# Kernel tuning notes

Measured on AMD Instinct MI355X. Metric: run time of the kernel, lower is better.

Reference implementation:

```python
import jax, jax.numpy as jnp
import numpy as np

EPS = 1e-5
TAU = 2.0
HEADS = 8
SCALE = 0.125


def _bn(y, g, b, m, v):
    # y: [TB, C, N]; per-channel eval-mode batchnorm
    inv = jax.lax.rsqrt(v + EPS)
    return (y - m[:, None]) * (g * inv)[:, None] + b[:, None]


def _lif(x_seq, vth):
    # spikingjelly MultiStepLIFNode: v += (x - v)/tau, spike = H(v - vth), hard reset v*(1-s)
    def step(mem, xt):
        mem = mem + (xt - mem) / TAU
        s = (mem >= vth).astype(xt.dtype)
        mem = mem * (1.0 - s)
        return mem, s
    _, spikes = jax.lax.scan(step, jnp.zeros_like(x_seq[0]), x_seq)
    return spikes


def setup_inputs() -> dict:
    key = jax.random.key(0)
    ks = jax.random.split(key, 8)
    T, B, C, H, W = 4, 16, 256, 32, 32
    d = {
        'x': jax.random.normal(ks[0], (T, B, C, H, W), jnp.float32),
        'res_attn': jnp.zeros((1,), jnp.float32),
    }
    for i, p in enumerate(['q', 'k', 'v']):
        d[p + '_w'] = jax.random.normal(ks[1 + i], (C, C), jnp.float32) * 0.02
        d[p + '_gamma'] = jnp.ones((C,), jnp.float32)
        d[p + '_beta'] = jnp.zeros((C,), jnp.float32)
        d[p + '_mean'] = jnp.zeros((C,), jnp.float32)
        d[p + '_var'] = jnp.ones((C,), jnp.float32)
    d['p_w'] = jax.random.normal(ks[4], (C, C), jnp.float32) * 0.02
    d['p_b'] = jnp.zeros((C,), jnp.float32)
    d['p_gamma'] = jnp.ones((C,), jnp.float32)
    d['p_beta'] = jnp.zeros((C,), jnp.float32)
    d['p_mean'] = jnp.zeros((C,), jnp.float32)
    d['p_var'] = jnp.ones((C,), jnp.float32)
    return d


def reference(x, res_attn, q_w, q_gamma, q_beta, q_mean, q_var,
              k_w, k_gamma, k_beta, k_mean, k_var,
              v_w, v_gamma, v_beta, v_mean, v_var,
              p_w, p_b, p_gamma, p_beta, p_mean, p_var):
    T, B, C, H, W = x.shape
    N = H * W
    d = C // HEADS
    x2 = x.reshape(T * B, C, N)

    def branch(w, g, b, m, v):
        y = _bn(jnp.einsum('oc,bcn->bon', w, x2), g, b, m, v).reshape(T, B, C, N)
        s = _lif(y, 1.0)  # [T,B,C,N]
        # -> [T,B,heads,N,d]
        return s.transpose(0, 1, 3, 2).reshape(T, B, N, HEADS, d).transpose(0, 1, 3, 2, 4)

    q = branch(q_w, q_gamma, q_beta, q_mean, q_var)
    k = branch(k_w, k_gamma, k_beta, k_mean, k_var)
    v = branch(v_w, v_gamma, v_beta, v_mean, v_var)

    kv = jnp.einsum('tbhnd,tbhne->tbhde', k, v)      # [T,B,h,d,d]
    attn = jnp.einsum('tbhnd,tbhde->tbhne', q, kv) * SCALE  # [T,B,h,N,d]
    xa = attn.transpose(0, 1, 2, 4, 3).reshape(T, B, C, N)
    xa = _lif(xa, 0.5)

    y = _bn(jnp.einsum('oc,bcn->bon', p_w, xa.reshape(T * B, C, N)) + p_b[:, None],
            p_gamma, p_beta, p_mean, p_var)
    out = _lif(y.reshape(T, B, C, H, W), 1.0)
    return (out, v)
```

## Files before the change

kernel.cpp:

```cpp
#include <hip/hip_runtime.h>
#include <stdint.h>

typedef unsigned int u32;
typedef unsigned short ushort_t;

#define T_ 4
#define B_ 16
#define C_ 256
#define N_ 1024
#define CN (C_ * N_)
#define M_ELEMS (64 * C_ * N_)

#define OFF_S    0ull
#define OFF_XC   67108864ull
#define OFF_SC   67108864ull
#define OFF_KV   134217728ull
#define OFF_BNS  136314880ull
#define OFF_WC   136331264ull
#define OFF_WPC  137510912ull

typedef __attribute__((ext_vector_type(8))) short bf16x8;
typedef __attribute__((ext_vector_type(4))) float f32x4;

#define SWZ(c) (((c) & ~3) | (((c) & 3) ^ (((c) >> 2) & 3) ^ (((c) >> 4) & 3)))

__device__ __forceinline__ ushort_t f2bf(float f) {
  u32 u = __float_as_uint(f);
  u32 r = (u + 0x7FFFu + ((u >> 16) & 1u)) >> 16;
  return (ushort_t)r;
}
__device__ __forceinline__ float bf2f(ushort_t h) { return __uint_as_float((u32)h << 16); }

__device__ __forceinline__ void async_copy16(const void* g, void* l) {
  __builtin_amdgcn_global_load_lds(
      (const __attribute__((address_space(1))) u32*)g,
      (__attribute__((address_space(3))) u32*)l, 16, 0, 0);
}

__device__ __forceinline__ void mfma_grp(const ushort_t* Ap, int aoff,
                                         bf16x8 b0, bf16x8 b1, bf16x8 b2, bf16x8 b3,
                                         f32x4* acc) {
  bf16x8 a0 = *(const bf16x8*)&Ap[aoff + 0 * 16 * 32];
  bf16x8 a1 = *(const bf16x8*)&Ap[aoff + 1 * 16 * 32];
  bf16x8 a2 = *(const bf16x8*)&Ap[aoff + 2 * 16 * 32];
  bf16x8 a3 = *(const bf16x8*)&Ap[aoff + 3 * 16 * 32];
  acc[0]  = __builtin_amdgcn_mfma_f32_16x16x32_bf16(a0, b0, acc[0],  0, 0, 0);
  acc[1]  = __builtin_amdgcn_mfma_f32_16x16x32_bf16(a0, b1, acc[1],  0, 0, 0);
  acc[2]  = __builtin_amdgcn_mfma_f32_16x16x32_bf16(a0, b2, acc[2],  0, 0, 0);
  acc[3]  = __builtin_amdgcn_mfma_f32_16x16x32_bf16(a0, b3, acc[3],  0, 0, 0);
  acc[4]  = __builtin_amdgcn_mfma_f32_16x16x32_bf16(a1, b0, acc[4],  0, 0, 0);
  acc[5]  = __builtin_amdgcn_mfma_f32_16x16x32_bf16(a1, b1, acc[5],  0, 0, 0);
  acc[6]  = __builtin_amdgcn_mfma_f32_16x16x32_bf16(a1, b2, acc[6],  0, 0, 0);
  acc[7]  = __builtin_amdgcn_mfma_f32_16x16x32_bf16(a1, b3, acc[7],  0, 0, 0);
  acc[8]  = __builtin_amdgcn_mfma_f32_16x16x32_bf16(a2, b0, acc[8],  0, 0, 0);
  acc[9]  = __builtin_amdgcn_mfma_f32_16x16x32_bf16(a2, b1, acc[9],  0, 0, 0);
  acc[10] = __builtin_amdgcn_mfma_f32_16x16x32_bf16(a2, b2, acc[10], 0, 0, 0);
  acc[11] = __builtin_amdgcn_mfma_f32_16x16x32_bf16(a2, b3, acc[11], 0, 0, 0);
  acc[12] = __builtin_amdgcn_mfma_f32_16x16x32_bf16(a3, b0, acc[12], 0, 0, 0);
  acc[13] = __builtin_amdgcn_mfma_f32_16x16x32_bf16(a3, b1, acc[13], 0, 0, 0);
  acc[14] = __builtin_amdgcn_mfma_f32_16x16x32_bf16(a3, b2, acc[14], 0, 0, 0);
  acc[15] = __builtin_amdgcn_mfma_f32_16x16x32_bf16(a3, b3, acc[15], 0, 0, 0);
}

__global__ void bn_prep(const float* __restrict__ qg, const float* __restrict__ qb2, const float* __restrict__ qm, const float* __restrict__ qv,
                        const float* __restrict__ kg, const float* __restrict__ kb, const float* __restrict__ km, const float* __restrict__ kvv,
                        const float* __restrict__ vg, const float* __restrict__ vb, const float* __restrict__ vm, const float* __restrict__ vv,
                        const float* __restrict__ pbias,
                        const float* __restrict__ pg, const float* __restrict__ pbt, const float* __restrict__ pm, const float* __restrict__ pv,
                        float* __restrict__ bns) {
  int i = threadIdx.x;
  int br = i >> 8, c = i & 255;
  const float *g, *bt, *m, *v;
  float bias = 0.f;
  if (br == 0)      { g = qg; bt = qb2; m = qm; v = qv; }
  else if (br == 1) { g = kg; bt = kb;  m = km; v = kvv; }
  else if (br == 2) { g = vg; bt = vb;  m = vm; v = vv; }
  else              { g = pg; bt = pbt; m = pm; v = pv; bias = pbias[c]; }
  float sc = g[c] / sqrtf(v[c] + 1e-5f);
  float sh = bt[c] + (bias - m[c]) * sc;
  float rcp = (sc != 0.f) ? (1.f / sc) : 0.f;
  *(float4*)&bns[4 * i] = make_float4(sc, sh, rcp, 0.f);
}

__global__ __launch_bounds__(256) void convert_w(const float* __restrict__ qw, const float* __restrict__ kw,
                                                 const float* __restrict__ vw, const float* __restrict__ pw,
                                                 ushort_t* __restrict__ Wc, ushort_t* __restrict__ Wpc) {
  int id = blockIdx.x * 256 + threadIdx.x;
  int br = id >> 16, o = (id >> 8) & 255, c = id & 255;
  const float* w = (br == 0) ? qw : (br == 1) ? kw : (br == 2) ? vw : pw;
  float f = w[o * 256 + c];
  ushort_t hi = f2bf(f);
  ushort_t lo = f2bf(f - bf2f(hi));
  if (br < 3) {
    ushort_t* d = Wc + (size_t)br * 196608 + (size_t)o * 768 + c;
    d[0] = hi; d[256] = lo; d[512] = hi;
  } else {
    ushort_t* d = Wpc + (size_t)o * 512 + c;
    d[0] = hi; d[256] = lo;
  }
}

__global__ __launch_bounds__(256) void convert_x(const float* __restrict__ x, ushort_t* __restrict__ Xc) {
  __shared__ ushort_t hi[32][260];
  __shared__ ushort_t lo[32][260];
  int bid = blockIdx.x;
  int nc = bid & 3, kb = (bid >> 2) & 7, tb = bid >> 5;
  int t = threadIdx.x;
  int n0 = nc * 256;
  const float* xb = x + (size_t)tb * CN + (size_t)(kb * 32) * N_ + n0;
#pragma unroll
  for (int p = 0; p < 8; ++p) {
    int k = p * 4 + (t >> 6);
    int n4 = (t & 63) * 4;
    float4 v = *(const float4*)&xb[(size_t)k * N_ + n4];
    ushort_t h0 = f2bf(v.x), h1 = f2bf(v.y), h2 = f2bf(v.z), h3 = f2bf(v.w);
    short4 hv = make_short4((short)h0, (short)h1, (short)h2, (short)h3);
    short4 lv = make_short4((short)f2bf(v.x - bf2f(h0)), (short)f2bf(v.y - bf2f(h1)),
                            (short)f2bf(v.z - bf2f(h2)), (short)f2bf(v.w - bf2f(h3)));
    *(short4*)&hi[k][n4] = hv;
    *(short4*)&lo[k][n4] = lv;
  }
  __syncthreads();
  ushort_t* Hs = Xc + ((size_t)(tb * 16 + kb) * 1024 + n0) * 32;
  ushort_t* Ls = Xc + ((size_t)(tb * 16 + 8 + kb) * 1024 + n0) * 32;
  int kq = t & 3;
#pragma unroll
  for (int q = 0; q < 4; ++q) {
    int n = q * 64 + (t >> 2);
    u32 a0 = (u32)hi[kq * 8 + 0][n] | ((u32)hi[kq * 8 + 1][n] << 16);
    u32 a1 = (u32)hi[kq * 8 + 2][n] | ((u32)hi[kq * 8 + 3][n] << 16);
    u32 a2 = (u32)hi[kq * 8 + 4][n] | ((u32)hi[kq * 8 + 5][n] << 16);
    u32 a3 = (u32)hi[kq * 8 + 6][n] | ((u32)hi[kq * 8 + 7][n] << 16);
    *(uint4*)(Hs + (size_t)n * 32 + kq * 8) = make_uint4(a0, a1, a2, a3);
    u32 b0 = (u32)lo[kq * 8 + 0][n] | ((u32)lo[kq * 8 + 1][n] << 16);
    u32 b1 = (u32)lo[kq * 8 + 2][n] | ((u32)lo[kq * 8 + 3][n] << 16);
    u32 b2 = (u32)lo[kq * 8 + 4][n] | ((u32)lo[kq * 8 + 5][n] << 16);
    u32 b3 = (u32)lo[kq * 8 + 6][n] | ((u32)lo[kq * 8 + 7][n] << 16);
    *(uint4*)(Ls + (size_t)n * 32 + kq * 8) = make_uint4(b0, b1, b2, b3);
  }
}

__global__ __launch_bounds__(256, 3) void gemm_qkv_lif(
    const ushort_t* __restrict__ Wc, const ushort_t* __restrict__ Xc,
    const float* __restrict__ bns, uint8_t* __restrict__ S) {
  __shared__ ushort_t Ah[2][4096];
  __shared__ ushort_t Xl[2][4096];
  __shared__ ushort_t Bh[2][4096];
  const int nt = blockIdx.x, mt = blockIdx.y, b = blockIdx.z;
  const int br = mt >> 1, rh = mt & 1;
  const ushort_t* Ab = Wc + (size_t)br * 196608 + (size_t)(rh * 128) * 768;
  const int tid = threadIdx.x;
  const int lane = tid & 63;
  const int quad = lane >> 4, r = lane & 15;
  const int w = tid >> 6;
  const int moff = (w & 1) * 64, noff = (w >> 1) * 64;
  const int c0 = tid, c1 = tid + 256;
  const int s0 = SWZ(c0), s1 = SWZ(c1);
  const int qx = quad ^ (r & 3) ^ ((r >> 2) & 3);
  const int aoff = (moff + r) * 32 + qx * 8;
  const int boff = (noff + r) * 32 + qx * 8;

  f32x4 acc[16];
#pragma unroll
  for (int f = 0; f < 16; ++f) acc[f] = (f32x4){0.f, 0.f, 0.f, 0.f};

  for (int t = 0; t < 4; ++t) {
    const ushort_t* Xtb = Xc + (size_t)(t * 16 + b) * 16 * 32768 + (size_t)(nt * 128) * 32;
    for (int p = 0; p < 4; ++p) {
      const ushort_t* AcH = Ab + p * 64;
      const ushort_t* AcL = Ab + 256 + p * 64;
      const ushort_t* Bh0 = Xtb + (size_t)(2 * p) * 32768;
      const ushort_t* Bh1 = Bh0 + 32768;
      async_copy16(AcH + (size_t)(c0 >> 2) * 768 + (s0 & 3) * 8,      &Ah[0][c0 * 8]);
      async_copy16(AcH + (size_t)(c1 >> 2) * 768 + (s1 & 3) * 8,      &Ah[0][c1 * 8]);
      async_copy16(AcH + (size_t)(c0 >> 2) * 768 + 32 + (s0 & 3) * 8, &Ah[1][c0 * 8]);
      async_copy16(AcH + (size_t)(c1 >> 2) * 768 + 32 + (s1 & 3) * 8, &Ah[1][c1 * 8]);
      async_copy16(AcL + (size_t)(c0 >> 2) * 768 + (s0 & 3) * 8,      &Xl[0][c0 * 8]);
      async_copy16(AcL + (size_t)(c1 >> 2) * 768 + (s1 & 3) * 8,      &Xl[0][c1 * 8]);
      async_copy16(AcL + (size_t)(c0 >> 2) * 768 + 32 + (s0 & 3) * 8, &Xl[1][c0 * 8]);
      async_copy16(AcL + (size_t)(c1 >> 2) * 768 + 32 + (s1 & 3) * 8, &Xl[1][c1 * 8]);
      async_copy16(Bh0 + s0 * 8, &Bh[0][c0 * 8]);
      async_copy16(Bh0 + s1 * 8, &Bh[0][c1 * 8]);
      async_copy16(Bh1 + s0 * 8, &Bh[1][c0 * 8]);
      async_copy16(Bh1 + s1 * 8, &Bh[1][c1 * 8]);
      __syncthreads();
      {
        bf16x8 b0 = *(const bf16x8*)&Bh[0][boff + 0 * 16 * 32];
        bf16x8 b1 = *(const bf16x8*)&Bh[0][boff + 1 * 16 * 32];
        bf16x8 b2 = *(const bf16x8*)&Bh[0][boff + 2 * 16 * 32];
        bf16x8 b3 = *(const bf16x8*)&Bh[0][boff + 3 * 16 * 32];
        mfma_grp(&Ah[0][0], aoff, b0, b1, b2, b3, acc);
        mfma_grp(&Xl[0][0], aoff, b0, b1, b2, b3, acc);
      }
      {
        bf16x8 b0 = *(const bf16x8*)&Bh[1][boff + 0 * 16 * 32];
        bf16x8 b1 = *(const bf16x8*)&Bh[1][boff + 1 * 16 * 32];
        bf16x8 b2 = *(const bf16x8*)&Bh[1][boff + 2 * 16 * 32];
        bf16x8 b3 = *(const bf16x8*)&Bh[1][boff + 3 * 16 * 32];
        mfma_grp(&Ah[1][0], aoff, b0, b1, b2, b3, acc);
        mfma_grp(&Xl[1][0], aoff, b0, b1, b2, b3, acc);
      }
      __syncthreads();
      const ushort_t* Bl0 = Xtb + (size_t)(8 + 2 * p) * 32768;
      const ushort_t* Bl1 = Bl0 + 32768;
      async_copy16(Bl0 + s0 * 8, &Xl[0][c0 * 8]);
      async_copy16(Bl0 + s1 * 8, &Xl[0][c1 * 8]);
      async_copy16(Bl1 + s0 * 8, &Xl[1][c0 * 8]);
      async_copy16(Bl1 + s1 * 8, &Xl[1][c1 * 8]);
      __syncthreads();
      {
        bf16x8 b0 = *(const bf16x8*)&Xl[0][boff + 0 * 16 * 32];
        bf16x8 b1 = *(const bf16x8*)&Xl[0][boff + 1 * 16 * 32];
        bf16x8 b2 = *(const bf16x8*)&Xl[0][boff + 2 * 16 * 32];
        bf16x8 b3 = *(const bf16x8*)&Xl[0][boff + 3 * 16 * 32];
        mfma_grp(&Ah[0][0], aoff, b0, b1, b2, b3, acc);
      }
      {
        bf16x8 b0 = *(const bf16x8*)&Xl[1][boff + 0 * 16 * 32];
        bf16x8 b1 = *(const bf16x8*)&Xl[1][boff + 1 * 16 * 32];
        bf16x8 b2 = *(const bf16x8*)&Xl[1][boff + 2 * 16 * 32];
        bf16x8 b3 = *(const bf16x8*)&Xl[1][boff + 3 * 16 * 32];
        mfma_grp(&Ah[1][0], aoff, b0, b1, b2, b3, acc);
      }
      __syncthreads();
    }
    uint8_t* Sb = S + (size_t)br * M_ELEMS + (size_t)(t * 16 + b) * CN;
#pragma unroll
    for (int i = 0; i < 4; ++i) {
#pragma unroll
      for (int rg = 0; rg < 4; ++rg) {
        int c = rh * 128 + moff + i * 16 + quad * 4 + rg;
        float4 bn = *(const float4*)&bns[4 * (br * 256 + c)];
        float hsc = 0.5f * bn.x;
        float hsh = 0.5f * bn.y;
        float rcp = bn.z;
        uint8_t* row = Sb + (size_t)c * N_ + nt * 128 + noff + r;
#pragma unroll
        for (int j = 0; j < 4; ++j) {
          float m = acc[i * 4 + j][rg] * hsc + hsh;
          uint8_t s = (m >= 1.0f) ? 1 : 0;
          row[j * 16] = s;
          acc[i * 4 + j][rg] = s ? 0.f : m * rcp;
        }
      }
    }
  }
}

__global__ __launch_bounds__(256) void kv_gram_tv(const uint8_t* __restrict__ SK,
                                                  const uint8_t* __restrict__ SV,
                                                  float* __restrict__ KV,
                                                  float* __restrict__ vout) {
  __shared__ unsigned long long Kb[32][17];
  __shared__ unsigned long long Vb[32][17];
  const int tb = blockIdx.x >> 3, h = blockIdx.x & 7;
  const uint8_t* K = SK + (size_t)tb * CN + (size_t)h * 32 * N_;
  const uint8_t* V = SV + (size_t)tb * CN + (size_t)h * 32 * N_;
  const int tid = threadIdx.x;
  const int row = tid >> 3, c8 = tid & 7;
  uint8_t* Kb8 = (uint8_t*)&Kb[row][0];
  uint8_t* Vb8 = (uint8_t*)&Vb[row][0];
#pragma unroll
  for (int i = 0; i < 16; ++i) {
    int c = c8 + 8 * i;
    unsigned long long xk = *(const unsigned long long*)(K + (size_t)row * N_ + (size_t)c * 8);
    unsigned long long xv = *(const unsigned long long*)(V + (size_t)row * N_ + (size_t)c * 8);
    Kb8[c] = (uint8_t)((xk * 0x8040201008040201ull) >> 56);
    Vb8[c] = (uint8_t)((xv * 0x8040201008040201ull) >> 56);
  }
  __syncthreads();
  {
    const int dd = tid >> 3, e0 = (tid & 7) * 4;
    int a0 = 0, a1 = 0, a2 = 0, a3 = 0;
#pragma unroll
    for (int c = 0; c < 16; ++c) {
      unsigned long long kd = Kb[dd][c];
      a0 += __popcll(kd & Vb[e0 + 0][c]);
      a1 += __popcll(kd & Vb[e0 + 1][c]);
      a2 += __popcll(kd & Vb[e0 + 2][c]);
      a3 += __popcll(kd & Vb[e0 + 3][c]);
    }
    float* o = KV + (size_t)(tb * 8 + h) * 1024 + dd * 32 + e0;
    o[0] = (float)a0; o[1] = (float)a1; o[2] = (float)a2; o[3] = (float)a3;
  }
  float* vo = vout + ((size_t)tb * 8 + h) * (size_t)(1024 * 32);
  const int sn = tid >> 3;
  const int dd0 = (tid & 7) * 4;
#pragma unroll 4
  for (int it = 0; it < 32; ++it) {
    int n = it * 32 + sn;
    int wi = n >> 6;
    int bit = ((n >> 3) & 7) * 8 + 7 - (n & 7);
    float4 v4;
    v4.x = ((Vb[dd0 + 0][wi] >> bit) & 1ull) ? 1.0f : 0.0f;
    v4.y = ((Vb[dd0 + 1][wi] >> bit) & 1ull) ? 1.0f : 0.0f;
    v4.z = ((Vb[dd0 + 2][wi] >> bit) & 1ull) ? 1.0f : 0.0f;
    v4.w = ((Vb[dd0 + 3][wi] >> bit) & 1ull) ? 1.0f : 0.0f;
    *(float4*)(vo + (size_t)n * 32 + dd0) = v4;
  }
}

__global__ __launch_bounds__(256) void attn_lif(const uint8_t* __restrict__ SQ,
                                                const float* __restrict__ KV,
                                                ushort_t* __restrict__ Sc) {
  __shared__ float kvs[1024];
  const int bid = blockIdx.x;
  const int nb = bid & 15, h = (bid >> 4) & 7, b = bid >> 7;
  const int n0 = nb * 64;
  const int tid = threadIdx.x;
  const int nl = tid & 63, eg = tid >> 6;
  float mem[8];
#pragma unroll
  for (int j = 0; j < 8; ++j) mem[j] = 0.f;
  for (int t = 0; t < 4; ++t) {
    const float* kvp = KV + (size_t)((t * B_ + b) * 8 + h) * 1024;
    *(float4*)&kvs[tid * 4] = *(const float4*)&kvp[tid * 4];
    __syncthreads();
    const uint8_t* q = SQ + (size_t)(t * B_ + b) * CN + (size_t)h * 32 * N_ + n0 + nl;
    float val[8];
#pragma unroll
    for (int j = 0; j < 8; ++j) val[j] = 0.f;
#pragma unroll 4
    for (int dd = 0; dd < 32; ++dd) {
      float qv = (float)q[(size_t)dd * N_];
      float4 ka = *(const float4*)&kvs[dd * 32 + eg * 8];
      float4 kb2 = *(const float4*)&kvs[dd * 32 + eg * 8 + 4];
      val[0] += qv * ka.x;  val[1] += qv * ka.y;  val[2] += qv * ka.z;  val[3] += qv * ka.w;
      val[4] += qv * kb2.x; val[5] += qv * kb2.y; val[6] += qv * kb2.z; val[7] += qv * kb2.w;
    }
    ushort_t pk[8];
#pragma unroll
    for (int j = 0; j < 8; ++j) {
      float a = val[j] * 0.125f;
      mem[j] += (a - mem[j]) * 0.5f;
      int s = (mem[j] >= 0.5f);
      pk[j] = s ? (ushort_t)0x3F80 : (ushort_t)0;
      if (s) mem[j] = 0.f;
    }
    uint4 o;
    o.x = (u32)pk[0] | ((u32)pk[1] << 16);
    o.y = (u32)pk[2] | ((u32)pk[3] << 16);
    o.z = (u32)pk[4] | ((u32)pk[5] << 16);
    o.w = (u32)pk[6] | ((u32)pk[7] << 16);
    *(uint4*)(Sc + ((size_t)((t * B_ + b) * 8 + h) * 1024 + n0 + nl) * 32 + eg * 8) = o;
    __syncthreads();
  }
}

__global__ __launch_bounds__(256, 3) void gemm_p_lif(
    const ushort_t* __restrict__ Wpc, const ushort_t* __restrict__ Sc,
    const float* __restrict__ bns, float* __restrict__ out) {
  __shared__ ushort_t Ah[2][4096];
  __shared__ ushort_t Al[2][4096];
  __shared__ ushort_t Bs[2][4096];
  const int nt = blockIdx.x, mt = blockIdx.y, b = blockIdx.z;
  const ushort_t* Ab = Wpc + (size_t)(mt * 128) * 512;
  const int tid = threadIdx.x;
  const int lane = tid & 63;
  const int quad = lane >> 4, r = lane & 15;
  const int w = tid >> 6;
  const int moff = (w & 1) * 64, noff = (w >> 1) * 64;
  const int c0 = tid, c1 = tid + 256;
  const int s0 = SWZ(c0), s1 = SWZ(c1);
  const int qx = quad ^ (r & 3) ^ ((r >> 2) & 3);
  const int aoff = (moff + r) * 32 + qx * 8;
  const int boff = (noff + r) * 32 + qx * 8;
  f32x4 acc[16];
#pragma unroll
  for (int f = 0; f < 16; ++f) acc[f] = (f32x4){0.f, 0.f, 0.f, 0.f};

  for (int t = 0; t < 4; ++t) {
    const ushort_t* Stb = Sc + (size_t)(t * 16 + b) * 8 * 32768 + (size_t)(nt * 128) * 32;
    for (int p = 0; p < 4; ++p) {
      const ushort_t* AcH = Ab + p * 64;
      const ushort_t* AcL = Ab + 256 + p * 64;
      const ushort_t* Bb0 = Stb + (size_t)(2 * p) * 32768;
      const ushort_t* Bb1 = Bb0 + 32768;
      async_copy16(AcH + (size_t)(c0 >> 2) * 512 + (s0 & 3) * 8,      &Ah[0][c0 * 8]);
      async_copy16(AcH + (size_t)(c1 >> 2) * 512 + (s1 & 3) * 8,      &Ah[0][c1 * 8]);
      async_copy16(AcH + (size_t)(c0 >> 2) * 512 + 32 + (s0 & 3) * 8, &Ah[1][c0 * 8]);
      async_copy16(AcH + (size_t)(c1 >> 2) * 512 + 32 + (s1 & 3) * 8, &Ah[1][c1 * 8]);
      async_copy16(AcL + (size_t)(c0 >> 2) * 512 + (s0 & 3) * 8,      &Al[0][c0 * 8]);
      async_copy16(AcL + (size_t)(c1 >> 2) * 512 + (s1 & 3) * 8,      &Al[0][c1 * 8]);
      async_copy16(AcL + (size_t)(c0 >> 2) * 512 + 32 + (s0 & 3) * 8, &Al[1][c0 * 8]);
      async_copy16(AcL + (size_t)(c1 >> 2) * 512 + 32 + (s1 & 3) * 8, &Al[1][c1 * 8]);
      async_copy16(Bb0 + s0 * 8, &Bs[0][c0 * 8]);
      async_copy16(Bb0 + s1 * 8, &Bs[0][c1 * 8]);
      async_copy16(Bb1 + s0 * 8, &Bs[1][c0 * 8]);
      async_copy16(Bb1 + s1 * 8, &Bs[1][c1 * 8]);
      __syncthreads();
      {
        bf16x8 b0 = *(const bf16x8*)&Bs[0][boff + 0 * 16 * 32];
        bf16x8 b1 = *(const bf16x8*)&Bs[0][boff + 1 * 16 * 32];
        bf16x8 b2 = *(const bf16x8*)&Bs[0][boff + 2 * 16 * 32];
        bf16x8 b3 = *(const bf16x8*)&Bs[0][boff + 3 * 16 * 32];
        mfma_grp(&Ah[0][0], aoff, b0, b1, b2, b3, acc);
        mfma_grp(&Al[0][0], aoff, b0, b1, b2, b3, acc);
      }
      {
        bf16x8 b0 = *(const bf16x8*)&Bs[1][boff + 0 * 16 * 32];
        bf16x8 b1 = *(const bf16x8*)&Bs[1][boff + 1 * 16 * 32];
        bf16x8 b2 = *(const bf16x8*)&Bs[1][boff + 2 * 16 * 32];
        bf16x8 b3 = *(const bf16x8*)&Bs[1][boff + 3 * 16 * 32];
        mfma_grp(&Ah[1][0], aoff, b0, b1, b2, b3, acc);
        mfma_grp(&Al[1][0], aoff, b0, b1, b2, b3, acc);
      }
      __syncthreads();
    }
    float* Ob = out + (size_t)(t * 16 + b) * CN;
#pragma unroll
    for (int i = 0; i < 4; ++i) {
#pragma unroll
      for (int rg = 0; rg < 4; ++rg) {
        int c = mt * 128 + moff + i * 16 + quad * 4 + rg;
        float4 bn = *(const float4*)&bns[4 * (768 + c)];
        float hsc = 0.5f * bn.x;
        float hsh = 0.5f * bn.y;
        float rcp = bn.z;
        float* row2 = Ob + (size_t)c * N_ + nt * 128 + noff + r;
#pragma unroll
        for (int j = 0; j < 4; ++j) {
          float m = acc[i * 4 + j][rg] * hsc + hsh;
          int s = (m >= 1.0f);
          row2[j * 16] = s ? 1.0f : 0.0f;
          acc[i * 4 + j][rg] = s ? 0.f : m * rcp;
        }
      }
    }
  }
}

extern "C" void kernel_launch(void* const* d_in, const int* in_sizes, int n_in,
                              void* d_out, int out_size, void* d_ws, size_t ws_size,
                              hipStream_t stream) {
  const float* x   = (const float*)d_in[0];
  const float* qw  = (const float*)d_in[2];
  const float* qg  = (const float*)d_in[3];
  const float* qb  = (const float*)d_in[4];
  const float* qm  = (const float*)d_in[5];
  const float* qv  = (const float*)d_in[6];
  const float* kw  = (const float*)d_in[7];
  const float* kg  = (const float*)d_in[8];
  const float* kb  = (const float*)d_in[9];
  const float* km  = (const float*)d_in[10];
  const float* kvv = (const float*)d_in[11];
  const float* vw  = (const float*)d_in[12];
  const float* vg  = (const float*)d_in[13];
  const float* vb  = (const float*)d_in[14];
  const float* vm  = (const float*)d_in[15];
  const float* vv  = (const float*)d_in[16];
  const float* pw  = (const float*)d_in[17];
  const float* pb  = (const float*)d_in[18];
  const float* pg  = (const float*)d_in[19];
  const float* pbt = (const float*)d_in[20];
  const float* pm  = (const float*)d_in[21];
  const float* pv  = (const float*)d_in[22];

  float* out = (float*)d_out;
  float* vout = out + M_ELEMS;

  uint8_t* ws = (uint8_t*)d_ws;
  uint8_t* S   = ws + OFF_S;
  ushort_t* Xc = (ushort_t*)(ws + OFF_XC);
  ushort_t* Sc = (ushort_t*)(ws + OFF_SC);
  float* KV    = (float*)(ws + OFF_KV);
  float* BNS   = (float*)(ws + OFF_BNS);
  ushort_t* Wc  = (ushort_t*)(ws + OFF_WC);
  ushort_t* Wpc = (ushort_t*)(ws + OFF_WPC);

  bn_prep<<<dim3(1), dim3(1024), 0, stream>>>(qg, qb, qm, qv, kg, kb, km, kvv,
                                              vg, vb, vm, vv, pb, pg, pbt, pm, pv, BNS);
  convert_w<<<dim3(1024), dim3(256), 0, stream>>>(qw, kw, vw, pw, Wc, Wpc);
  convert_x<<<dim3(2048), dim3(256), 0, stream>>>(x, Xc);
  gemm_qkv_lif<<<dim3(8, 6, 16), dim3(256), 0, stream>>>(Wc, Xc, BNS, S);
  kv_gram_tv<<<dim3(512), dim3(256), 0, stream>>>(S + 1ull * M_ELEMS, S + 2ull * M_ELEMS, KV, vout);
  attn_lif<<<dim3(2048), dim3(256), 0, stream>>>(S, KV, Sc);
  gemm_p_lif<<<dim3(8, 2, 16), dim3(256), 0, stream>>>(Wpc, Sc, BNS, out);
}
```

Baseline: 391.9 us.

## Load GEMM B operands directly from global into registers, merge prep kernels

In both MFMA GEMM kernels the B-operand (activation) tiles are now read straight from global memory into registers in the MFMA fragment layout instead of being staged through swizzled shared memory. This removes one LDS buffer and, in the QKV kernel, two extra barriers per k-step, and lets the global loads overlap with the MFMAs. The risk is less coalesced global access and no reuse of B across waves sharing the same columns. The bn_prep and convert_w kernels are also fused into one launch to save a kernel launch.

Measured after the change: 419.6 us. 7.1% more time.

```diff
diff --git a/kernel.cpp b/kernel.cpp
--- a/kernel.cpp
+++ b/kernel.cpp
@@ -62,41 +62,45 @@
   acc[15] = __builtin_amdgcn_mfma_f32_16x16x32_bf16(a3, b3, acc[15], 0, 0, 0);
 }
 
-__global__ void bn_prep(const float* __restrict__ qg, const float* __restrict__ qb2, const float* __restrict__ qm, const float* __restrict__ qv,
-                        const float* __restrict__ kg, const float* __restrict__ kb, const float* __restrict__ km, const float* __restrict__ kvv,
-                        const float* __restrict__ vg, const float* __restrict__ vb, const float* __restrict__ vm, const float* __restrict__ vv,
-                        const float* __restrict__ pbias,
-                        const float* __restrict__ pg, const float* __restrict__ pbt, const float* __restrict__ pm, const float* __restrict__ pv,
-                        float* __restrict__ bns) {
-  int i = threadIdx.x;
-  int br = i >> 8, c = i & 255;
-  const float *g, *bt, *m, *v;
-  float bias = 0.f;
-  if (br == 0)      { g = qg; bt = qb2; m = qm; v = qv; }
-  else if (br == 1) { g = kg; bt = kb;  m = km; v = kvv; }
-  else if (br == 2) { g = vg; bt = vb;  m = vm; v = vv; }
-  else              { g = pg; bt = pbt; m = pm; v = pv; bias = pbias[c]; }
-  float sc = g[c] / sqrtf(v[c] + 1e-5f);
-  float sh = bt[c] + (bias - m[c]) * sc;
-  float rcp = (sc != 0.f) ? (1.f / sc) : 0.f;
-  *(float4*)&bns[4 * i] = make_float4(sc, sh, rcp, 0.f);
-}
-
-__global__ __launch_bounds__(256) void convert_w(const float* __restrict__ qw, const float* __restrict__ kw,
-                                                 const float* __restrict__ vw, const float* __restrict__ pw,
-                                                 ushort_t* __restrict__ Wc, ushort_t* __restrict__ Wpc) {
-  int id = blockIdx.x * 256 + threadIdx.x;
-  int br = id >> 16, o = (id >> 8) & 255, c = id & 255;
-  const float* w = (br == 0) ? qw : (br == 1) ? kw : (br == 2) ? vw : pw;
-  float f = w[o * 256 + c];
-  ushort_t hi = f2bf(f);
-  ushort_t lo = f2bf(f - bf2f(hi));
-  if (br < 3) {
-    ushort_t* d = Wc + (size_t)br * 196608 + (size_t)o * 768 + c;
-    d[0] = hi; d[256] = lo; d[512] = hi;
+__global__ __launch_bounds__(256) void prep_w(
+    const float* __restrict__ qw, const float* __restrict__ kw,
+    const float* __restrict__ vw, const float* __restrict__ pw,
+    const float* __restrict__ qg, const float* __restrict__ qb2, const float* __restrict__ qm, const float* __restrict__ qv,
+    const float* __restrict__ kg, const float* __restrict__ kb, const float* __restrict__ km, const float* __restrict__ kvv,
+    const float* __restrict__ vg, const float* __restrict__ vb, const float* __restrict__ vm, const float* __restrict__ vv,
+    const float* __restrict__ pbias, const float* __restrict__ pg, const float* __restrict__ pbt,
+    const float* __restrict__ pm, const float* __restrict__ pv,
+    ushort_t* __restrict__ Wc, ushort_t* __restrict__ Wpc, float* __restrict__ bns) {
+  if (blockIdx.x < 1024) {
+    int id = blockIdx.x * 256 + threadIdx.x;
+    int br = id >> 16, o = (id >> 8) & 255, c = id & 255;
+    const float* w = (br == 0) ? qw : (br == 1) ? kw : (br == 2) ? vw : pw;
+    float f = w[o * 256 + c];
+    ushort_t hi = f2bf(f);
+    ushort_t lo = f2bf(f - bf2f(hi));
+    if (br < 3) {
+      ushort_t* d = Wc + (size_t)br * 196608 + (size_t)o * 768 + c;
+      d[0] = hi; d[256] = lo; d[512] = hi;
+    } else {
+      ushort_t* d = Wpc + (size_t)o * 512 + c;
+      d[0] = hi; d[256] = lo;
+    }
   } else {
-    ushort_t* d = Wpc + (size_t)o * 512 + c;
-    d[0] = hi; d[256] = lo;
+#pragma unroll
+    for (int rep = 0; rep < 4; ++rep) {
+      int i = rep * 256 + threadIdx.x;
+      int br = i >> 8, c = i & 255;
+      const float *g, *bt, *m, *v;
+      float bias = 0.f;
+      if (br == 0)      { g = qg; bt = qb2; m = qm; v = qv; }
+      else if (br == 1) { g = kg; bt = kb;  m = km; v = kvv; }
+      else if (br == 2) { g = vg; bt = vb;  m = vm; v = vv; }
+      else              { g = pg; bt = pbt; m = pm; v = pv; bias = pbias[c]; }
+      float sc = g[c] / sqrtf(v[c] + 1e-5f);
+      float sh = bt[c] + (bias - m[c]) * sc;
+      float rcp = (sc != 0.f) ? (1.f / sc) : 0.f;
+      *(float4*)&bns[4 * i] = make_float4(sc, sh, rcp, 0.f);
+    }
   }
 }
 
@@ -144,8 +148,7 @@
     const ushort_t* __restrict__ Wc, const ushort_t* __restrict__ Xc,
     const float* __restrict__ bns, uint8_t* __restrict__ S) {
   __shared__ ushort_t Ah[2][4096];
-  __shared__ ushort_t Xl[2][4096];
-  __shared__ ushort_t Bh[2][4096];
+  __shared__ ushort_t Al[2][4096];
   const int nt = blockIdx.x, mt = blockIdx.y, b = blockIdx.z;
   const int br = mt >> 1, rh = mt & 1;
   const ushort_t* Ab = Wc + (size_t)br * 196608 + (size_t)(rh * 128) * 768;
@@ -158,7 +161,7 @@
   const int s0 = SWZ(c0), s1 = SWZ(c1);
   const int qx = quad ^ (r & 3) ^ ((r >> 2) & 3);
   const int aoff = (moff + r) * 32 + qx * 8;
-  const int boff = (noff + r) * 32 + qx * 8;
+  const int bro = (noff + r) * 32 + quad * 8;
 
   f32x4 acc[16];
 #pragma unroll
@@ -169,59 +172,41 @@
     for (int p = 0; p < 4; ++p) {
       const ushort_t* AcH = Ab + p * 64;
       const ushort_t* AcL = Ab + 256 + p * 64;
-      const ushort_t* Bh0 = Xtb + (size_t)(2 * p) * 32768;
-      const ushort_t* Bh1 = Bh0 + 32768;
       async_copy16(AcH + (size_t)(c0 >> 2) * 768 + (s0 & 3) * 8,      &Ah[0][c0 * 8]);
       async_copy16(AcH + (size_t)(c1 >> 2) * 768 + (s1 & 3) * 8,      &Ah[0][c1 * 8]);
       async_copy16(AcH + (size_t)(c0 >> 2) * 768 + 32 + (s0 & 3) * 8, &Ah[1][c0 * 8]);
       async_copy16(AcH + (size_t)(c1 >> 2) * 768 + 32 + (s1 & 3) * 8, &Ah[1][c1 * 8]);
-      async_copy16(AcL + (size_t)(c0 >> 2) * 768 + (s0 & 3) * 8,      &Xl[0][c0 * 8]);
-      async_copy16(AcL + (size_t)(c1 >> 2) * 768 + (s1 & 3) * 8,      &Xl[0][c1 * 8]);
-      async_copy16(AcL + (size_t)(c0 >> 2) * 768 + 32 + (s0 & 3) * 8, &Xl[1][c0 * 8]);
-      async_copy16(AcL + (size_t)(c1 >> 2) * 768 + 32 + (s1 & 3) * 8, &Xl[1][c1 * 8]);
-      async_copy16(Bh0 + s0 * 8, &Bh[0][c0 * 8]);
-      async_copy16(Bh0 + s1 * 8, &Bh[0][c1 * 8]);
-      async_copy16(Bh1 + s0 * 8, &Bh[1][c0 * 8]);
-      async_copy16(Bh1 + s1 * 8, &Bh[1][c1 * 8]);
+      async_copy16(AcL + (size_t)(c0 >> 2) * 768 + (s0 & 3) * 8,      &Al[0][c0 * 8]);
+      async_copy16(AcL + (size_t)(c1 >> 2) * 768 + (s1 & 3) * 8,      &Al[0][c1 * 8]);
+      async_copy16(AcL + (size_t)(c0 >> 2) * 768 + 32 + (s0 & 3) * 8, &Al[1][c0 * 8]);
+      async_copy16(AcL + (size_t)(c1 >> 2) * 768 + 32 + (s1 & 3) * 8, &Al[1][c1 * 8]);
+      const ushort_t* B0 = Xtb + (size_t)(2 * p) * 32768 + bro;
+      const ushort_t* B1 = B0 + 32768;
+      const ushort_t* B2 = Xtb + (size_t)(8 + 2 * p) * 32768 + bro;
+      const ushort_t* B3 = B2 + 32768;
+      bf16x8 gA0 = *(const bf16x8*)(B0 + 0 * 512);
+      bf16x8 gA1 = *(const bf16x8*)(B0 + 1 * 512);
+      bf16x8 gA2 = *(const bf16x8*)(B0 + 2 * 512);
+      bf16x8 gA3 = *(const bf16x8*)(B0 + 3 * 512);
       __syncthreads();
-      {
-        bf16x8 b0 = *(const bf16x8*)&Bh[0][boff + 0 * 16 * 32];
-        bf16x8 b1 = *(const bf16x8*)&Bh[0][boff + 1 * 16 * 32];
-        bf16x8 b2 = *(const bf16x8*)&Bh[0][boff + 2 * 16 * 32];
-        bf16x8 b3 = *(const bf16x8*)&Bh[0][boff + 3 * 16 * 32];
-        mfma_grp(&Ah[0][0], aoff, b0, b1, b2, b3, acc);
-        mfma_grp(&Xl[0][0], aoff, b0, b1, b2, b3, acc);
-      }
-      {
-        bf16x8 b0 = *(const bf16x8*)&Bh[1][boff + 0 * 16 * 32];
-        bf16x8 b1 = *(const bf16x8*)&Bh[1][boff + 1 * 16 * 32];
-        bf16x8 b2 = *(const bf16x8*)&Bh[1][boff + 2 * 16 * 32];
-        bf16x8 b3 = *(const bf16x8*)&Bh[1][boff + 3 * 16 * 32];
-        mfma_grp(&Ah[1][0], aoff, b0, b1, b2, b3, acc);
-        mfma_grp(&Xl[1][0], aoff, b0, b1, b2, b3, acc);
-      }
-      __syncthreads();
-      const ushort_t* Bl0 = Xtb + (size_t)(8 + 2 * p) * 32768;
-      const ushort_t* Bl1 = Bl0 + 32768;
-      async_copy16(Bl0 + s0 * 8, &Xl[0][c0 * 8]);
-      async_copy16(Bl0 + s1 * 8, &Xl[0][c1 * 8]);
-      async_copy16(Bl1 + s0 * 8, &Xl[1][c0 * 8]);
-      async_copy16(Bl1 + s1 * 8, &Xl[1][c1 * 8]);
-      __syncthreads();
-      {
-        bf16x8 b0 = *(const bf16x8*)&Xl[0][boff + 0 * 16 * 32];
-        bf16x8 b1 = *(const bf16x8*)&Xl[0][boff + 1 * 16 * 32];
-        bf16x8 b2 = *(const bf16x8*)&Xl[0][boff + 2 * 16 * 32];
-        bf16x8 b3 = *(const bf16x8*)&Xl[0][boff + 3 * 16 * 32];
-        mfma_grp(&Ah[0][0], aoff, b0, b1, b2, b3, acc);
-      }
-      {
-        bf16x8 b0 = *(const bf16x8*)&Xl[1][boff + 0 * 16 * 32];
-        bf16x8 b1 = *(const bf16x8*)&Xl[1][boff + 1 * 16 * 32];
-        bf16x8 b2 = *(const bf16x8*)&Xl[1][boff + 2 * 16 * 32];
-        bf16x8 b3 = *(const bf16x8*)&Xl[1][boff + 3 * 16 * 32];
-        mfma_grp(&Ah[1][0], aoff, b0, b1, b2, b3, acc);
-      }
+      bf16x8 gB0 = *(const bf16x8*)(B1 + 0 * 512);
+      bf16x8 gB1 = *(const bf16x8*)(B1 + 1 * 512);
+      bf16x8 gB2 = *(const bf16x8*)(B1 + 2 * 512);
+      bf16x8 gB3 = *(const bf16x8*)(B1 + 3 * 512);
+      mfma_grp(&Ah[0][0], aoff, gA0, gA1, gA2, gA3, acc);
+      mfma_grp(&Al[0][0], aoff, gA0, gA1, gA2, gA3, acc);
+      gA0 = *(const bf16x8*)(B2 + 0 * 512);
+      gA1 = *(const bf16x8*)(B2 + 1 * 512);
+      gA2 = *(const bf16x8*)(B2 + 2 * 512);
+      gA3 = *(const bf16x8*)(B2 + 3 * 512);
+      mfma_grp(&Ah[1][0], aoff, gB0, gB1, gB2, gB3, acc);
+      mfma_grp(&Al[1][0], aoff, gB0, gB1, gB2, gB3, acc);
+      gB0 = *(const bf16x8*)(B3 + 0 * 512);
+      gB1 = *(const bf16x8*)(B3 + 1 * 512);
+      gB2 = *(const bf16x8*)(B3 + 2 * 512);
+      gB3 = *(const bf16x8*)(B3 + 3 * 512);
+      mfma_grp(&Ah[0][0], aoff, gA0, gA1, gA2, gA3, acc);
+      mfma_grp(&Ah[1][0], aoff, gB0, gB1, gB2, gB3, acc);
       __syncthreads();
     }
     uint8_t* Sb = S + (size_t)br * M_ELEMS + (size_t)(t * 16 + b) * CN;
@@ -352,7 +337,6 @@
     const float* __restrict__ bns, float* __restrict__ out) {
   __shared__ ushort_t Ah[2][4096];
   __shared__ ushort_t Al[2][4096];
-  __shared__ ushort_t Bs[2][4096];
   const int nt = blockIdx.x, mt = blockIdx.y, b = blockIdx.z;
   const ushort_t* Ab = Wpc + (size_t)(mt * 128) * 512;
   const int tid = threadIdx.x;
@@ -364,7 +348,7 @@
   const int s0 = SWZ(c0), s1 = SWZ(c1);
   const int qx = quad ^ (r & 3) ^ ((r >> 2) & 3);
   const int aoff = (moff + r) * 32 + qx * 8;
-  const int boff = (noff + r) * 32 + qx * 8;
+  const int bro = (noff + r) * 32 + quad * 8;
   f32x4 acc[16];
 #pragma unroll
   for (int f = 0; f < 16; ++f) acc[f] = (f32x4){0.f, 0.f, 0.f, 0.f};
@@ -374,8 +358,6 @@
     for (int p = 0; p < 4; ++p) {
       const ushort_t* AcH = Ab + p * 64;
       const ushort_t* AcL = Ab + 256 + p * 64;
-      const ushort_t* Bb0 = Stb + (size_t)(2 * p) * 32768;
-      const ushort_t* Bb1 = Bb0 + 32768;
       async_copy16(AcH + (size_t)(c0 >> 2) * 512 + (s0 & 3) * 8,      &Ah[0][c0 * 8]);
       async_copy16(AcH + (size_t)(c1 >> 2) * 512 + (s1 & 3) * 8,      &Ah[0][c1 * 8]);
       async_copy16(AcH + (size_t)(c0 >> 2) * 512 + 32 + (s0 & 3) * 8, &Ah[1][c0 * 8]);
@@ -384,27 +366,21 @@
       async_copy16(AcL + (size_t)(c1 >> 2) * 512 + (s1 & 3) * 8,      &Al[0][c1 * 8]);
       async_copy16(AcL + (size_t)(c0 >> 2) * 512 + 32 + (s0 & 3) * 8, &Al[1][c0 * 8]);
       async_copy16(AcL + (size_t)(c1 >> 2) * 512 + 32 + (s1 & 3) * 8, &Al[1][c1 * 8]);
-      async_copy16(Bb0 + s0 * 8, &Bs[0][c0 * 8]);
-      async_copy16(Bb0 + s1 * 8, &Bs[0][c1 * 8]);
-      async_copy16(Bb1 + s0 * 8, &Bs[1][c0 * 8]);
-      async_copy16(Bb1 + s1 * 8, &Bs[1][c1 * 8]);
+      const ushort_t* B0 = Stb + (size_t)(2 * p) * 32768 + bro;
+      const ushort_t* B1 = B0 + 32768;
+      bf16x8 gA0 = *(const bf16x8*)(B0 + 0 * 512);
+      bf16x8 gA1 = *(const bf16x8*)(B0 + 1 * 512);
+      bf16x8 gA2 = *(const bf16x8*)(B0 + 2 * 512);
+      bf16x8 gA3 = *(const bf16x8*)(B0 + 3 * 512);
       __syncthreads();
-      {
-        bf16x8 b0 = *(const bf16x8*)&Bs[0][boff + 0 * 16 * 32];
-        bf16x8 b1 = *(const bf16x8*)&Bs[0][boff + 1 * 16 * 32];
-        bf16x8 b2 = *(const bf16x8*)&Bs[0][boff + 2 * 16 * 32];
-        bf16x8 b3 = *(const bf16x8*)&Bs[0][boff + 3 * 16 * 32];
-        mfma_grp(&Ah[0][0], aoff, b0, b1, b2, b3, acc);
-        mfma_grp(&Al[0][0], aoff, b0, b1, b2, b3, acc);
-      }
-      {
-        bf16x8 b0 = *(const bf16x8*)&Bs[1][boff + 0 * 16 * 32];
-        bf16x8 b1 = *(const bf16x8*)&Bs[1][boff + 1 * 16 * 32];
-        bf16x8 b2 = *(const bf16x8*)&Bs[1][boff + 2 * 16 * 32];
-        bf16x8 b3 = *(const bf16x8*)&Bs[1][boff + 3 * 16 * 32];
-        mfma_grp(&Ah[1][0], aoff, b0, b1, b2, b3, acc);
-        mfma_grp(&Al[1][0], aoff, b0, b1, b2, b3, acc);
-      }
+      bf16x8 gB0 = *(const bf16x8*)(B1 + 0 * 512);
+      bf16x8 gB1 = *(const bf16x8*)(B1 + 1 * 512);
+      bf16x8 gB2 = *(const bf16x8*)(B1 + 2 * 512);
+      bf16x8 gB3 = *(const bf16x8*)(B1 + 3 * 512);
+      mfma_grp(&Ah[0][0], aoff, gA0, gA1, gA2, gA3, acc);
+      mfma_grp(&Al[0][0], aoff, gA0, gA1, gA2, gA3, acc);
+      mfma_grp(&Ah[1][0], aoff, gB0, gB1, gB2, gB3, acc);
+      mfma_grp(&Al[1][0], aoff, gB0, gB1, gB2, gB3, acc);
       __syncthreads();
     }
     float* Ob = out + (size_t)(t * 16 + b) * CN;
@@ -468,9 +444,10 @@
   ushort_t* Wc  = (ushort_t*)(ws + OFF_WC);
   ushort_t* Wpc = (ushort_t*)(ws + OFF_WPC);
 
-  bn_prep<<<dim3(1), dim3(1024), 0, stream>>>(qg, qb, qm, qv, kg, kb, km, kvv,
-                                              vg, vb, vm, vv, pb, pg, pbt, pm, pv, BNS);
-  convert_w<<<dim3(1024), dim3(256), 0, stream>>>(qw, kw, vw, pw, Wc, Wpc);
+  prep_w<<<dim3(1025), dim3(256), 0, stream>>>(qw, kw, vw, pw,
+                                               qg, qb, qm, qv, kg, kb, km, kvv,
+                                               vg, vb, vm, vv, pb, pg, pbt, pm, pv,
+                                               Wc, Wpc, BNS);
   convert_x<<<dim3(2048), dim3(256), 0, stream>>>(x, Xc);
   gemm_qkv_lif<<<dim3(8, 6, 16), dim3(256), 0, stream>>>(Wc, Xc, BNS, S);
   kv_gram_tv<<<dim3(512), dim3(256), 0, stream>>>(S + 1ull * M_ELEMS, S + 2ull * M_ELEMS, KV, vout);
```
